# Performance work log

Hardware: AMD Instinct MI355X
Metric: run time of the kernel (lower is better)

## Reference

```python
import jax, jax.numpy as jnp
import numpy as np

VOCAB, EMSIZE, NBINS = 50000, 300, 5
B, Q, D, L = 32, 16, 10, 1000
EPS = 1e-8
# numpy.histogram edges from self.bins = [-1.0, -0.5, 0, 0.5, 1.0, 1.0]
BIN_LO = np.array([-1.0, -0.5, 0.0, 0.5, 1.0], np.float32)
BIN_HI = np.array([-0.5, 0.0, 0.5, 1.0, 1.0], np.float32)


def setup_inputs() -> dict:
    key = jax.random.key(0)
    ks = jax.random.split(key, 12)
    return {
        "batch_queries": jax.random.randint(ks[0], (B, Q), 0, VOCAB),
        "batch_docs": jax.random.randint(ks[1], (B, D, L), 0, VOCAB),
        "embedding": jax.random.normal(ks[2], (VOCAB, EMSIZE), jnp.float32) * 0.1,
        "gate_w": jax.random.normal(ks[3], (1, EMSIZE), jnp.float32) * 0.05,
        "gate_b": jnp.zeros((1,), jnp.float32),
        "w1": jax.random.normal(ks[4], (1, NBINS), jnp.float32) * 0.3,
        "b1": jnp.zeros((1,), jnp.float32),
        "w2": jax.random.normal(ks[5], (1, 1), jnp.float32),
        "b2": jnp.zeros((1,), jnp.float32),
        "out_w": jax.random.normal(ks[6], (1, 1), jnp.float32),
        "out_b": jnp.zeros((1,), jnp.float32),
    }


def _histogram(cos):  # cos: [B, D, Q, L] -> counts [B, D, Q, NBINS]
    lo = jnp.asarray(BIN_LO)
    hi = jnp.asarray(BIN_HI)
    c = cos[..., None]  # [B, D, Q, L, 1]
    # bins 0..3 half-open [lo, hi); last bin closed [1.0, 1.0]
    in_bin = (c >= lo) & (c < hi)
    last = (c[..., -1] >= lo[-1]) & (c[..., -1] <= hi[-1])
    in_bin = in_bin.at[..., -1].set(last)
    return in_bin.astype(jnp.float32).sum(axis=-2)


def reference(batch_queries, batch_docs, embedding, gate_w, gate_b,
              w1, b1, w2, b2, out_w, out_b):
    emb_q = embedding[batch_queries]            # [B, Q, E]
    emb_d = embedding[batch_docs]               # [B, D, L, E]

    # gating network: Linear(E,1) then softmax over query terms
    gate_logits = jnp.einsum('bqe,oe->bq', emb_q, gate_w) + gate_b[0]
    term_weights = jax.nn.softmax(gate_logits, axis=-1)  # [B, Q]

    # cosine similarity between every query term and doc term
    w12 = jnp.einsum('bqe,bdle->bdql', emb_q, emb_d)     # [B, D, Q, L]
    nq = jnp.linalg.norm(emb_q, axis=-1)                 # [B, Q]
    nd = jnp.linalg.norm(emb_d, axis=-1)                 # [B, D, L]
    denom = jnp.maximum(nq[:, None, :, None] * nd[:, :, None, :], EPS)
    cos = w12 / denom                                    # [B, D, Q, L]

    hist = _histogram(cos)                               # [B, D, Q, NBINS]

    # ffnn: Linear(NBINS,1) -> Linear(1,1)
    h = jnp.einsum('bdqn,on->bdq', hist, w1) + b1[0]
    ffnn_out = h * w2[0, 0] + b2[0]                      # [B, D, Q]

    weighted = ffnn_out * term_weights[:, None, :]       # [B, D, Q]
    pooled = weighted.sum(axis=-1)                       # [B, D]
    score = pooled * out_w[0, 0] + out_b[0]
    return score                                         # [B, D]
```

## Files before the change

### kernel.cpp

```cpp
#include <hip/hip_runtime.h>
#include <hip/hip_fp16.h>
#include <math.h>

#define VOCAB_ 50000
#define B_ 32
#define Q_ 16
#define D_ 10
#define L_ 1000
#define E_ 300

#define NS_  4
#define TPS_ 250
#define RP_  304
#define G8_  38

typedef unsigned short u16x8 __attribute__((ext_vector_type(8)));

__global__ __launch_bounds__(256) void drmm_cvt(
    const float* __restrict__ emb, unsigned short* __restrict__ emb16)
{
    const int row = blockIdx.x;
    const int tid = threadIdx.x;
    const float* src = emb + (size_t)row * E_;
    unsigned short* dst = emb16 + (size_t)row * RP_;
    dst[tid] = (tid < E_) ? __half_as_ushort(__float2half_rn(src[tid]))
                          : (unsigned short)0;
    if (tid < RP_ - 256) {
        const int c = 256 + tid;
        dst[c] = (c < E_) ? __half_as_ushort(__float2half_rn(src[c]))
                          : (unsigned short)0;
    }
}

__global__ __launch_bounds__(256) void drmm_prep(
    const int* __restrict__ bq, const float* __restrict__ emb,
    const float* __restrict__ gate_w, const float* __restrict__ gate_b,
    const float* __restrict__ b1, const float* __restrict__ w2,
    const float* __restrict__ b2, const float* __restrict__ out_w,
    const float* __restrict__ out_b,
    float* __restrict__ wqBuf, float* __restrict__ nqBuf,
    float* __restrict__ score)
{
    const int b = blockIdx.x;
    const int tid = threadIdx.x;
    const int w = tid >> 6, lane = tid & 63;
    __shared__ float logits[Q_];

#pragma unroll
    for (int i = 0; i < 4; ++i) {
        const int q = w * 4 + i;
        const int tok = bq[b * Q_ + q];
        const float* row = emb + (size_t)tok * E_;
        float4 dv = *(const float4*)(row + 4 * lane);
        float4 gv = *(const float4*)(gate_w + 4 * lane);
        float pd = dv.x * gv.x + dv.y * gv.y + dv.z * gv.z + dv.w * gv.w;
        float ps = dv.x * dv.x + dv.y * dv.y + dv.z * dv.z + dv.w * dv.w;
        if (lane < 11) {
            float4 dv2 = *(const float4*)(row + 256 + 4 * lane);
            float4 gv2 = *(const float4*)(gate_w + 256 + 4 * lane);
            pd += dv2.x * gv2.x + dv2.y * gv2.y + dv2.z * gv2.z + dv2.w * gv2.w;
            ps += dv2.x * dv2.x + dv2.y * dv2.y + dv2.z * dv2.z + dv2.w * dv2.w;
        }
#pragma unroll
        for (int off = 32; off > 0; off >>= 1) {
            pd += __shfl_xor(pd, off);
            ps += __shfl_xor(ps, off);
        }
        if (lane == 0) {
            logits[q] = pd + gate_b[0];
            nqBuf[b * Q_ + q] = sqrtf(ps);
        }
    }
    __syncthreads();

    if (tid == 0) {
        float m = -1e30f;
        for (int q = 0; q < Q_; ++q) m = fmaxf(m, logits[q]);
        float e[Q_];
        float s = 0.f;
        for (int q = 0; q < Q_; ++q) { e[q] = expf(logits[q] - m); s += e[q]; }
        const float sc = out_w[0] * w2[0] / s;
        for (int q = 0; q < Q_; ++q) wqBuf[b * Q_ + q] = e[q] * sc;
    }
    if (tid < D_)
        score[b * D_ + tid] = out_w[0] * (w2[0] * b1[0] + b2[0]) + out_b[0];
}

template<bool F16>
__global__ __launch_bounds__(256, 4) void drmm_main(
    const int* __restrict__ bq, const int* __restrict__ bdocs,
    const float* __restrict__ emb, const unsigned short* __restrict__ emb16,
    const float* __restrict__ w1,
    const float* __restrict__ wqBuf, const float* __restrict__ nqBuf,
    float* __restrict__ score)
{
    const int ls = blockIdx.x;
    const int d  = blockIdx.y;
    const int b  = blockIdx.z;
    const int tid  = threadIdx.x;
    const int lane = tid & 63;
    const int w    = tid >> 6;

    __shared__ float4 qt[Q_ * 76];
    __shared__ float wsum[4];

    for (int u = tid; u < Q_ * 76; u += 256) {
        const int q = u / 76;
        const int c = u - q * 76;
        float4 v = make_float4(0.f, 0.f, 0.f, 0.f);
        if (c < 75)
            v = *(const float4*)(emb + (size_t)bq[b * Q_ + q] * E_ + 4 * c);
        qt[u] = v;
    }
    __syncthreads();

    const int tok = bdocs[(b * D_ + d) * L_ + ls * TPS_ + min(tid, TPS_ - 1)];

    float acc[Q_];
#pragma unroll
    for (int q = 0; q < Q_; ++q) acc[q] = 0.f;
    float sqA = 0.f, sqB = 0.f;

    if constexpr (F16) {
        const unsigned short* drow = emb16 + (size_t)tok * RP_;
#pragma unroll 10
        for (int g = 0; g < G8_; ++g) {
            const u16x8 dv = *(const u16x8*)(drow + 8 * g);
            const float d0 = __half2float(__ushort_as_half(dv[0]));
            const float d1 = __half2float(__ushort_as_half(dv[1]));
            const float d2 = __half2float(__ushort_as_half(dv[2]));
            const float d3 = __half2float(__ushort_as_half(dv[3]));
            const float d4 = __half2float(__ushort_as_half(dv[4]));
            const float d5 = __half2float(__ushort_as_half(dv[5]));
            const float d6 = __half2float(__ushort_as_half(dv[6]));
            const float d7 = __half2float(__ushort_as_half(dv[7]));
            sqA = fmaf(d0, d0, fmaf(d2, d2, fmaf(d4, d4, fmaf(d6, d6, sqA))));
            sqB = fmaf(d1, d1, fmaf(d3, d3, fmaf(d5, d5, fmaf(d7, d7, sqB))));
#pragma unroll
            for (int q = 0; q < Q_; ++q) {
                const float4 qa = qt[q * 76 + 2 * g];
                const float4 qb = qt[q * 76 + 2 * g + 1];
                float t0 = fmaf(d0, qa.x, fmaf(d1, qa.y,
                           fmaf(d2, qa.z, fmaf(d3, qa.w, acc[q]))));
                acc[q]   = fmaf(d4, qb.x, fmaf(d5, qb.y,
                           fmaf(d6, qb.z, fmaf(d7, qb.w, t0))));
            }
        }
    } else {
        const float* drow = emb + (size_t)tok * E_;
#pragma unroll 9
        for (int g = 0; g < 37; ++g) {
            const float4 a  = *(const float4*)(drow + 8 * g);
            const float4 c4 = *(const float4*)(drow + 8 * g + 4);
            sqA = fmaf(a.x, a.x, fmaf(a.z, a.z, fmaf(c4.x, c4.x, fmaf(c4.z, c4.z, sqA))));
            sqB = fmaf(a.y, a.y, fmaf(a.w, a.w, fmaf(c4.y, c4.y, fmaf(c4.w, c4.w, sqB))));
#pragma unroll
            for (int q = 0; q < Q_; ++q) {
                const float4 qa = qt[q * 76 + 2 * g];
                const float4 qb = qt[q * 76 + 2 * g + 1];
                float t0 = fmaf(a.x, qa.x, fmaf(a.y, qa.y,
                           fmaf(a.z, qa.z, fmaf(a.w, qa.w, acc[q]))));
                acc[q]   = fmaf(c4.x, qb.x, fmaf(c4.y, qb.y,
                           fmaf(c4.z, qb.z, fmaf(c4.w, qb.w, t0))));
            }
        }
        {
            const float4 a = *(const float4*)(drow + 296);
            sqA = fmaf(a.x, a.x, fmaf(a.z, a.z, sqA));
            sqB = fmaf(a.y, a.y, fmaf(a.w, a.w, sqB));
#pragma unroll
            for (int q = 0; q < Q_; ++q) {
                const float4 qa = qt[q * 76 + 74];
                acc[q] = fmaf(a.x, qa.x, fmaf(a.y, qa.y,
                         fmaf(a.z, qa.z, fmaf(a.w, qa.w, acc[q]))));
            }
        }
    }

    float total = 0.f;
    if (tid < TPS_) {
        const float nd = sqrtf(sqA + sqB);
        const float w10 = w1[0], w11 = w1[1], w12 = w1[2],
                    w13 = w1[3], w14 = w1[4];
#pragma unroll
        for (int q = 0; q < Q_; ++q) {
            const float nqv = nqBuf[b * Q_ + q];
            const float wqv = wqBuf[b * Q_ + q];
            const float denom = fmaxf(nqv * nd, 1e-8f);
            const float a = acc[q];
            const float wv = (a < -denom)        ? 0.f
                           : (a < -0.5f * denom) ? w10
                           : (a < 0.f)           ? w11
                           : (a < 0.5f * denom)  ? w12
                           : (a < denom)         ? w13
                           : (a <= denom)        ? w14
                                                 : 0.f;
            total = fmaf(wqv, wv, total);
        }
    }

#pragma unroll
    for (int off = 32; off > 0; off >>= 1) total += __shfl_xor(total, off);
    if (lane == 0) wsum[w] = total;
    __syncthreads();
    if (tid == 0)
        atomicAdd(&score[b * D_ + d], wsum[0] + wsum[1] + wsum[2] + wsum[3]);
}

extern "C" void kernel_launch(void* const* d_in, const int* in_sizes, int n_in,
                              void* d_out, int out_size, void* d_ws, size_t ws_size,
                              hipStream_t stream)
{
    const int*   bq     = (const int*)d_in[0];
    const int*   bdocs  = (const int*)d_in[1];
    const float* emb    = (const float*)d_in[2];
    const float* gate_w = (const float*)d_in[3];
    const float* gate_b = (const float*)d_in[4];
    const float* w1     = (const float*)d_in[5];
    const float* b1     = (const float*)d_in[6];
    const float* w2     = (const float*)d_in[7];
    const float* b2     = (const float*)d_in[8];
    const float* out_w  = (const float*)d_in[9];
    const float* out_b  = (const float*)d_in[10];

    float* score = (float*)d_out;
    float* wqBuf = (float*)d_ws;
    float* nqBuf = wqBuf + B_ * Q_;

    const size_t e16_off   = 4096;
    const size_t e16_bytes = (size_t)VOCAB_ * RP_ * sizeof(unsigned short);
    const bool useF16 = ws_size >= e16_off + e16_bytes;
    unsigned short* emb16 = (unsigned short*)((char*)d_ws + e16_off);

    if (useF16)
        drmm_cvt<<<dim3(VOCAB_), dim3(256), 0, stream>>>(emb, emb16);

    drmm_prep<<<dim3(B_), dim3(256), 0, stream>>>(
        bq, emb, gate_w, gate_b, b1, w2, b2, out_w, out_b, wqBuf, nqBuf, score);

    if (useF16)
        drmm_main<true><<<dim3(NS_, D_, B_), dim3(256), 0, stream>>>(
            bq, bdocs, emb, emb16, w1, wqBuf, nqBuf, score);
    else
        drmm_main<false><<<dim3(NS_, D_, B_), dim3(256), 0, stream>>>(
            bq, bdocs, emb, emb16, w1, wqBuf, nqBuf, score);
}
```

Baseline: 219.7 us.

## Use packed fp16 dot2 for similarity and vectorize embedding conversion

The fp16 main kernel now keeps both query and doc vectors in half precision and accumulates with v_dot2 (fp16 pairs into an fp32 accumulator), cutting the number of VALU ops and the per-element conversions. Query tiles in shared memory are stored as fp16, which halves LDS traffic. The conversion kernel is rewritten so each thread converts 8 floats with vector loads and stores, replacing one block per row. The trade-off is that query values are now rounded to fp16 as well, which can move cosine values that sit near bin edges.

```diff
diff --git a/kernel.cpp b/kernel.cpp
--- a/kernel.cpp
+++ b/kernel.cpp
@@ -13,23 +13,43 @@
 #define TPS_ 250
 #define RP_  304
 #define G8_  38
-
-typedef unsigned short u16x8 __attribute__((ext_vector_type(8)));
+#define CVU_ (VOCAB_ * G8_)
+
+typedef _Float16 half8 __attribute__((ext_vector_type(8)));
+typedef _Float16 h2_t  __attribute__((ext_vector_type(2)));
+
+#if __has_builtin(__builtin_amdgcn_fdot2)
+#define DOT2(a, b, c) __builtin_amdgcn_fdot2((a), (b), (c), false)
+#else
+#define DOT2(a, b, c) fmaf((float)(a)[0], (float)(b)[0], \
+                      fmaf((float)(a)[1], (float)(b)[1], (c)))
+#endif
+#define SV2(v, i) __builtin_shufflevector((v), (v), 2*(i), 2*(i)+1)
 
 __global__ __launch_bounds__(256) void drmm_cvt(
-    const float* __restrict__ emb, unsigned short* __restrict__ emb16)
-{
-    const int row = blockIdx.x;
-    const int tid = threadIdx.x;
-    const float* src = emb + (size_t)row * E_;
-    unsigned short* dst = emb16 + (size_t)row * RP_;
-    dst[tid] = (tid < E_) ? __half_as_ushort(__float2half_rn(src[tid]))
-                          : (unsigned short)0;
-    if (tid < RP_ - 256) {
-        const int c = 256 + tid;
-        dst[c] = (c < E_) ? __half_as_ushort(__float2half_rn(src[c]))
-                          : (unsigned short)0;
-    }
+    const float* __restrict__ emb, _Float16* __restrict__ emb16)
+{
+    const int u = blockIdx.x * 256 + threadIdx.x;
+    if (u >= CVU_) return;
+    const int row = u / G8_;
+    const int g   = u - row * G8_;
+    const float* src = emb + (size_t)row * E_ + 8 * g;
+    half8 o;
+    if (g < 37) {
+        const float4 a = *(const float4*)src;
+        const float4 c = *(const float4*)(src + 4);
+        o[0] = (_Float16)a.x; o[1] = (_Float16)a.y;
+        o[2] = (_Float16)a.z; o[3] = (_Float16)a.w;
+        o[4] = (_Float16)c.x; o[5] = (_Float16)c.y;
+        o[6] = (_Float16)c.z; o[7] = (_Float16)c.w;
+    } else {
+        const float4 a = *(const float4*)src;
+        o[0] = (_Float16)a.x; o[1] = (_Float16)a.y;
+        o[2] = (_Float16)a.z; o[3] = (_Float16)a.w;
+        o[4] = (_Float16)0.f; o[5] = (_Float16)0.f;
+        o[6] = (_Float16)0.f; o[7] = (_Float16)0.f;
+    }
+    *(half8*)(emb16 + (size_t)row * RP_ + 8 * g) = o;
 }
 
 __global__ __launch_bounds__(256) void drmm_prep(
@@ -86,11 +106,9 @@
         score[b * D_ + tid] = out_w[0] * (w2[0] * b1[0] + b2[0]) + out_b[0];
 }
 
-template<bool F16>
-__global__ __launch_bounds__(256, 4) void drmm_main(
+__global__ __launch_bounds__(256, 4) void drmm_main_f16(
     const int* __restrict__ bq, const int* __restrict__ bdocs,
-    const float* __restrict__ emb, const unsigned short* __restrict__ emb16,
-    const float* __restrict__ w1,
+    const _Float16* __restrict__ emb16, const float* __restrict__ w1,
     const float* __restrict__ wqBuf, const float* __restrict__ nqBuf,
     float* __restrict__ score)
 {
@@ -101,85 +119,43 @@
     const int lane = tid & 63;
     const int w    = tid >> 6;
 
-    __shared__ float4 qt[Q_ * 76];
+    __shared__ half8 qt[Q_ * G8_];
     __shared__ float wsum[4];
 
-    for (int u = tid; u < Q_ * 76; u += 256) {
-        const int q = u / 76;
-        const int c = u - q * 76;
-        float4 v = make_float4(0.f, 0.f, 0.f, 0.f);
-        if (c < 75)
-            v = *(const float4*)(emb + (size_t)bq[b * Q_ + q] * E_ + 4 * c);
-        qt[u] = v;
+    for (int u = tid; u < Q_ * G8_; u += 256) {
+        const int q = u / G8_;
+        const int g = u - q * G8_;
+        qt[u] = *(const half8*)(emb16 + (size_t)bq[b * Q_ + q] * RP_ + 8 * g);
     }
     __syncthreads();
 
     const int tok = bdocs[(b * D_ + d) * L_ + ls * TPS_ + min(tid, TPS_ - 1)];
+    const _Float16* drow = emb16 + (size_t)tok * RP_;
 
     float acc[Q_];
 #pragma unroll
     for (int q = 0; q < Q_; ++q) acc[q] = 0.f;
-    float sqA = 0.f, sqB = 0.f;
-
-    if constexpr (F16) {
-        const unsigned short* drow = emb16 + (size_t)tok * RP_;
-#pragma unroll 10
-        for (int g = 0; g < G8_; ++g) {
-            const u16x8 dv = *(const u16x8*)(drow + 8 * g);
-            const float d0 = __half2float(__ushort_as_half(dv[0]));
-            const float d1 = __half2float(__ushort_as_half(dv[1]));
-            const float d2 = __half2float(__ushort_as_half(dv[2]));
-            const float d3 = __half2float(__ushort_as_half(dv[3]));
-            const float d4 = __half2float(__ushort_as_half(dv[4]));
-            const float d5 = __half2float(__ushort_as_half(dv[5]));
-            const float d6 = __half2float(__ushort_as_half(dv[6]));
-            const float d7 = __half2float(__ushort_as_half(dv[7]));
-            sqA = fmaf(d0, d0, fmaf(d2, d2, fmaf(d4, d4, fmaf(d6, d6, sqA))));
-            sqB = fmaf(d1, d1, fmaf(d3, d3, fmaf(d5, d5, fmaf(d7, d7, sqB))));
-#pragma unroll
-            for (int q = 0; q < Q_; ++q) {
-                const float4 qa = qt[q * 76 + 2 * g];
-                const float4 qb = qt[q * 76 + 2 * g + 1];
-                float t0 = fmaf(d0, qa.x, fmaf(d1, qa.y,
-                           fmaf(d2, qa.z, fmaf(d3, qa.w, acc[q]))));
-                acc[q]   = fmaf(d4, qb.x, fmaf(d5, qb.y,
-                           fmaf(d6, qb.z, fmaf(d7, qb.w, t0))));
-            }
-        }
-    } else {
-        const float* drow = emb + (size_t)tok * E_;
-#pragma unroll 9
-        for (int g = 0; g < 37; ++g) {
-            const float4 a  = *(const float4*)(drow + 8 * g);
-            const float4 c4 = *(const float4*)(drow + 8 * g + 4);
-            sqA = fmaf(a.x, a.x, fmaf(a.z, a.z, fmaf(c4.x, c4.x, fmaf(c4.z, c4.z, sqA))));
-            sqB = fmaf(a.y, a.y, fmaf(a.w, a.w, fmaf(c4.y, c4.y, fmaf(c4.w, c4.w, sqB))));
-#pragma unroll
-            for (int q = 0; q < Q_; ++q) {
-                const float4 qa = qt[q * 76 + 2 * g];
-                const float4 qb = qt[q * 76 + 2 * g + 1];
-                float t0 = fmaf(a.x, qa.x, fmaf(a.y, qa.y,
-                           fmaf(a.z, qa.z, fmaf(a.w, qa.w, acc[q]))));
-                acc[q]   = fmaf(c4.x, qb.x, fmaf(c4.y, qb.y,
-                           fmaf(c4.z, qb.z, fmaf(c4.w, qb.w, t0))));
-            }
-        }
-        {
-            const float4 a = *(const float4*)(drow + 296);
-            sqA = fmaf(a.x, a.x, fmaf(a.z, a.z, sqA));
-            sqB = fmaf(a.y, a.y, fmaf(a.w, a.w, sqB));
-#pragma unroll
-            for (int q = 0; q < Q_; ++q) {
-                const float4 qa = qt[q * 76 + 74];
-                acc[q] = fmaf(a.x, qa.x, fmaf(a.y, qa.y,
-                         fmaf(a.z, qa.z, fmaf(a.w, qa.w, acc[q]))));
-            }
+    float sq = 0.f;
+
+#pragma unroll 8
+    for (int g = 0; g < G8_; ++g) {
+        const half8 dv = *(const half8*)(drow + 8 * g);
+        const h2_t d0 = SV2(dv, 0), d1 = SV2(dv, 1),
+                   d2 = SV2(dv, 2), d3 = SV2(dv, 3);
+        sq = DOT2(d0, d0, DOT2(d1, d1, DOT2(d2, d2, DOT2(d3, d3, sq))));
+#pragma unroll
+        for (int q = 0; q < Q_; ++q) {
+            const half8 qv = qt[q * G8_ + g];
+            float t = DOT2(SV2(qv, 0), d0, acc[q]);
+            t       = DOT2(SV2(qv, 1), d1, t);
+            t       = DOT2(SV2(qv, 2), d2, t);
+            acc[q]  = DOT2(SV2(qv, 3), d3, t);
         }
     }
 
     float total = 0.f;
     if (tid < TPS_) {
-        const float nd = sqrtf(sqA + sqB);
+        const float nd = sqrtf(sq);
         const float w10 = w1[0], w11 = w1[1], w12 = w1[2],
                     w13 = w1[3], w14 = w1[4];
 #pragma unroll
@@ -207,6 +183,98 @@
         atomicAdd(&score[b * D_ + d], wsum[0] + wsum[1] + wsum[2] + wsum[3]);
 }
 
+__global__ __launch_bounds__(256, 4) void drmm_main_f32(
+    const int* __restrict__ bq, const int* __restrict__ bdocs,
+    const float* __restrict__ emb, const float* __restrict__ w1,
+    const float* __restrict__ wqBuf, const float* __restrict__ nqBuf,
+    float* __restrict__ score)
+{
+    const int ls = blockIdx.x;
+    const int d  = blockIdx.y;
+    const int b  = blockIdx.z;
+    const int tid  = threadIdx.x;
+    const int lane = tid & 63;
+    const int w    = tid >> 6;
+
+    __shared__ float4 qt[Q_ * 76];
+    __shared__ float wsum[4];
+
+    for (int u = tid; u < Q_ * 76; u += 256) {
+        const int q = u / 76;
+        const int c = u - q * 76;
+        float4 v = make_float4(0.f, 0.f, 0.f, 0.f);
+        if (c < 75)
+            v = *(const float4*)(emb + (size_t)bq[b * Q_ + q] * E_ + 4 * c);
+        qt[u] = v;
+    }
+    __syncthreads();
+
+    const int tok = bdocs[(b * D_ + d) * L_ + ls * TPS_ + min(tid, TPS_ - 1)];
+    const float* drow = emb + (size_t)tok * E_;
+
+    float acc[Q_];
+#pragma unroll
+    for (int q = 0; q < Q_; ++q) acc[q] = 0.f;
+    float sqA = 0.f, sqB = 0.f;
+
+#pragma unroll 9
+    for (int g = 0; g < 37; ++g) {
+        const float4 a  = *(const float4*)(drow + 8 * g);
+        const float4 c4 = *(const float4*)(drow + 8 * g + 4);
+        sqA = fmaf(a.x, a.x, fmaf(a.z, a.z, fmaf(c4.x, c4.x, fmaf(c4.z, c4.z, sqA))));
+        sqB = fmaf(a.y, a.y, fmaf(a.w, a.w, fmaf(c4.y, c4.y, fmaf(c4.w, c4.w, sqB))));
+#pragma unroll
+        for (int q = 0; q < Q_; ++q) {
+            const float4 qa = qt[q * 76 + 2 * g];
+            const float4 qb = qt[q * 76 + 2 * g + 1];
+            float t0 = fmaf(a.x, qa.x, fmaf(a.y, qa.y,
+                       fmaf(a.z, qa.z, fmaf(a.w, qa.w, acc[q]))));
+            acc[q]   = fmaf(c4.x, qb.x, fmaf(c4.y, qb.y,
+                       fmaf(c4.z, qb.z, fmaf(c4.w, qb.w, t0))));
+        }
+    }
+    {
+        const float4 a = *(const float4*)(drow + 296);
+        sqA = fmaf(a.x, a.x, fmaf(a.z, a.z, sqA));
+        sqB = fmaf(a.y, a.y, fmaf(a.w, a.w, sqB));
+#pragma unroll
+        for (int q = 0; q < Q_; ++q) {
+            const float4 qa = qt[q * 76 + 74];
+            acc[q] = fmaf(a.x, qa.x, fmaf(a.y, qa.y,
+                     fmaf(a.z, qa.z, fmaf(a.w, qa.w, acc[q]))));
+        }
+    }
+
+    float total = 0.f;
+    if (tid < TPS_) {
+        const float nd = sqrtf(sqA + sqB);
+        const float w10 = w1[0], w11 = w1[1], w12 = w1[2],
+                    w13 = w1[3], w14 = w1[4];
+#pragma unroll
+        for (int q = 0; q < Q_; ++q) {
+            const float nqv = nqBuf[b * Q_ + q];
+            const float wqv = wqBuf[b * Q_ + q];
+            const float denom = fmaxf(nqv * nd, 1e-8f);
+            const float a = acc[q];
+            const float wv = (a < -denom)        ? 0.f
+                           : (a < -0.5f * denom) ? w10
+                           : (a < 0.f)           ? w11
+                           : (a < 0.5f * denom)  ? w12
+                           : (a < denom)         ? w13
+                           : (a <= denom)        ? w14
+                                                 : 0.f;
+            total = fmaf(wqv, wv, total);
+        }
+    }
+
+#pragma unroll
+    for (int off = 32; off > 0; off >>= 1) total += __shfl_xor(total, off);
+    if (lane == 0) wsum[w] = total;
+    __syncthreads();
+    if (tid == 0)
+        atomicAdd(&score[b * D_ + d], wsum[0] + wsum[1] + wsum[2] + wsum[3]);
+}
+
 extern "C" void kernel_launch(void* const* d_in, const int* in_sizes, int n_in,
                               void* d_out, int out_size, void* d_ws, size_t ws_size,
                               hipStream_t stream)
@@ -228,20 +296,20 @@
     float* nqBuf = wqBuf + B_ * Q_;
 
     const size_t e16_off   = 4096;
-    const size_t e16_bytes = (size_t)VOCAB_ * RP_ * sizeof(unsigned short);
+    const size_t e16_bytes = (size_t)VOCAB_ * RP_ * sizeof(_Float16);
     const bool useF16 = ws_size >= e16_off + e16_bytes;
-    unsigned short* emb16 = (unsigned short*)((char*)d_ws + e16_off);
+    _Float16* emb16 = (_Float16*)((char*)d_ws + e16_off);
 
     if (useF16)
-        drmm_cvt<<<dim3(VOCAB_), dim3(256), 0, stream>>>(emb, emb16);
+        drmm_cvt<<<dim3((CVU_ + 255) / 256), dim3(256), 0, stream>>>(emb, emb16);
 
     drmm_prep<<<dim3(B_), dim3(256), 0, stream>>>(
         bq, emb, gate_w, gate_b, b1, w2, b2, out_w, out_b, wqBuf, nqBuf, score);
 
     if (useF16)
-        drmm_main<true><<<dim3(NS_, D_, B_), dim3(256), 0, stream>>>(
-            bq, bdocs, emb, emb16, w1, wqBuf, nqBuf, score);
+        drmm_main_f16<<<dim3(NS_, D_, B_), dim3(256), 0, stream>>>(
+            bq, bdocs, emb16, w1, wqBuf, nqBuf, score);
     else
-        drmm_main<false><<<dim3(NS_, D_, B_), dim3(256), 0, stream>>>(
-            bq, bdocs, emb, emb16, w1, wqBuf, nqBuf, score);
-}
+        drmm_main_f32<<<dim3(NS_, D_, B_), dim3(256), 0, stream>>>(
+            bq, bdocs, emb, w1, wqBuf, nqBuf, score);
+}
```

Result: faster. 188.0 us (-14.4%).
